# Kernel optimization log

Hardware: AMD Instinct MI355X
Metric: run time of the kernel (lower is better)

Reference implementation:

```python
import jax, jax.numpy as jnp
import numpy as np


def setup_inputs() -> dict:
    key = jax.random.key(0)
    kx, kq, kk, kv = jax.random.split(key, 4)
    B, S, D_IN, H, D_OUT = 2, 2048, 768, 12, 64
    scale = 0.02
    return {
        "x": jax.random.normal(kx, (B, S, D_IN), dtype=jnp.float32),
        "Wq": jax.random.normal(kq, (H, D_IN, D_OUT), dtype=jnp.float32) * scale,
        "Wk": jax.random.normal(kk, (H, D_IN, D_OUT), dtype=jnp.float32) * scale,
        "Wv": jax.random.normal(kv, (H, D_IN, D_OUT), dtype=jnp.float32) * scale,
    }


def reference(x, Wq, Wk, Wv):
    # x: [B, S, d_in]; Wq/Wk/Wv: [H, d_in, d_out] (stacked per-head Linear weights, no bias)
    B, S, _ = x.shape
    H, _, d_out = Wq.shape
    q = jnp.einsum("bsd,hde->bhse", x, Wq)  # [B, H, S, d_out]
    k = jnp.einsum("bsd,hde->bhse", x, Wk)
    v = jnp.einsum("bsd,hde->bhse", x, Wv)
    scores = jnp.einsum("bhse,bhte->bhst", q, k) / jnp.sqrt(jnp.float32(d_out))
    causal = jnp.tril(jnp.ones((S, S), dtype=bool))  # True = keep
    scores = jnp.where(causal, scores, jnp.float32(-jnp.inf))
    attn = jax.nn.softmax(scores, axis=-1)  # dropout = 0.0 -> identity
    ctx = jnp.einsum("bhst,bhte->bhse", attn, v)  # [B, H, S, d_out]
    # concat heads along last dim: [B, S, H*d_out]
    return ctx.transpose(0, 2, 1, 3).reshape(B, S, H * d_out)
```

## Files before the change

kernel.cpp:

```cpp
#include <hip/hip_runtime.h>
#include <hip/hip_bf16.h>


typedef short bf16x8 __attribute__((ext_vector_type(8)));
typedef short bf16x4 __attribute__((ext_vector_type(4)));
typedef float f32x4  __attribute__((ext_vector_type(4)));

#define MFMA16(a, b, c)  __builtin_amdgcn_mfma_f32_16x16x32_bf16((a), (b), (c), 0, 0, 0)
#define MFMAK16(a, b, c) __builtin_amdgcn_mfma_f32_16x16x16bf16_1k((a), (b), (c), 0, 0, 0)

static __device__ __forceinline__ unsigned short f2bf(float f) {
    unsigned int u = __builtin_bit_cast(unsigned int, f);
    u += 0x7fffu + ((u >> 16) & 1u);
    return (unsigned short)(u >> 16);
}

static __device__ __forceinline__ int sw(int row, int cb) {
    return (row << 7) + (cb ^ ((row & 7) << 4));
}

static __device__ __forceinline__ void gld16(const void* g, void* l) {
    __builtin_amdgcn_global_load_lds(
        (__attribute__((address_space(1))) void*)g,
        (__attribute__((address_space(3))) void*)l, 16, 0, 0);
}

__global__ __launch_bounds__(256) void prep(const float* __restrict__ x,
                                            const float* __restrict__ Wq,
                                            const float* __restrict__ Wk,
                                            const float* __restrict__ Wv,
                                            char* __restrict__ xb,
                                            char* __restrict__ wtb) {
    __shared__ float tile[64][65];
    const int bid = blockIdx.x;
    const int t = threadIdx.x;
    if (bid < 768) {
        const int stile = bid & 63, ks = bid >> 6;
        const int row = t >> 2, k16 = (t & 3) * 16;
        const float* src = x + (size_t)(stile * 64 + row) * 768 + ks * 64 + k16;
        char* img = xb + ((size_t)stile * 12 + ks) * 8192;
        const float4 v0 = *(const float4*)(src);
        const float4 v1 = *(const float4*)(src + 4);
        const float4 v2 = *(const float4*)(src + 8);
        const float4 v3 = *(const float4*)(src + 12);
        bf16x8 o0, o1;
        o0[0] = (short)f2bf(v0.x); o0[1] = (short)f2bf(v0.y);
        o0[2] = (short)f2bf(v0.z); o0[3] = (short)f2bf(v0.w);
        o0[4] = (short)f2bf(v1.x); o0[5] = (short)f2bf(v1.y);
        o0[6] = (short)f2bf(v1.z); o0[7] = (short)f2bf(v1.w);
        o1[0] = (short)f2bf(v2.x); o1[1] = (short)f2bf(v2.y);
        o1[2] = (short)f2bf(v2.z); o1[3] = (short)f2bf(v2.w);
        o1[4] = (short)f2bf(v3.x); o1[5] = (short)f2bf(v3.y);
        o1[6] = (short)f2bf(v3.z); o1[7] = (short)f2bf(v3.w);
        *(bf16x8*)(img + sw(row, k16 * 2)) = o0;
        *(bf16x8*)(img + sw(row, k16 * 2 + 16)) = o1;
    } else {
        const int idx = bid - 768;
        const int wh = idx % 36, dt = idx / 36;
        const int w = wh / 12, h = wh % 12;
        const float* W = (w == 0) ? Wq : (w == 1) ? Wk : Wv;
        for (int i = 0; i < 4; ++i) {
            int c = t + i * 256;
            int d = c >> 4, e4 = (c & 15) * 4;
            const float4 v = *(const float4*)(W + (size_t)(h * 768 + dt * 64 + d) * 64 + e4);
            tile[d][e4 + 0] = v.x; tile[d][e4 + 1] = v.y;
            tile[d][e4 + 2] = v.z; tile[d][e4 + 3] = v.w;
        }
        __syncthreads();
        char* img = wtb + ((size_t)(wh * 12) + dt) * 8192;
        for (int i = 0; i < 4; ++i) {
            int c = t + i * 256;
            int e = c >> 4, d4 = (c & 15) * 4;
            ushort4 o;
            o.x = f2bf(tile[d4 + 0][e]); o.y = f2bf(tile[d4 + 1][e]);
            o.z = f2bf(tile[d4 + 2][e]); o.w = f2bf(tile[d4 + 3][e]);
            *(ushort4*)(img + e * 128 + ((d4 * 2) ^ ((e & 7) << 4))) = o;
        }
    }
}

__global__ __launch_bounds__(256) void proj_qkv(const char* __restrict__ xb,
                                                const char* __restrict__ wtb,
                                                unsigned short* __restrict__ q,
                                                unsigned short* __restrict__ ksw,
                                                char* __restrict__ vsw) {
    __shared__ __align__(16) char smem[65536];
    const int stile = blockIdx.x;
    const int h = blockIdx.y;
    const int t = threadIdx.x;
    const int wave = t >> 6, lane = t & 63;
    const int lhi = lane >> 4, llo = lane & 15;
    const int wr = wave >> 1, wc = wave & 1;

    const char* asrc = xb + (size_t)stile * 12 * 8192;

    f32x4 acc[3][2][2] = {};

    #define STAGE(KS, BUF)                                                       \
        do {                                                                     \
            const char* s0 = asrc + (KS) * 8192;                                 \
            char* d0 = smem + (BUF) * 32768;                                     \
            gld16(s0 + t * 16, d0 + t * 16);                                     \
            gld16(s0 + t * 16 + 4096, d0 + t * 16 + 4096);                       \
            for (int w3 = 0; w3 < 3; ++w3) {                                     \
                const char* s1 = wtb + ((size_t)((w3 * 12 + h) * 12) + (KS)) * 8192; \
                char* d1 = smem + (BUF) * 32768 + (1 + w3) * 8192;               \
                gld16(s1 + t * 16, d1 + t * 16);                                 \
                gld16(s1 + t * 16 + 4096, d1 + t * 16 + 4096);                   \
            }                                                                    \
        } while (0)

    STAGE(0, 0);
    __syncthreads();
    int cur = 0;
    for (int ks = 0; ks < 12; ++ks) {
        if (ks < 11) STAGE(ks + 1, cur ^ 1);
        char* Alds = smem + cur * 32768;
        #pragma unroll
        for (int kk = 0; kk < 2; ++kk) {
            bf16x8 a[2];
            #pragma unroll
            for (int m = 0; m < 2; ++m)
                a[m] = *(const bf16x8*)(Alds + sw(wr * 32 + m * 16 + llo, kk * 64 + lhi * 16));
            #pragma unroll
            for (int w3 = 0; w3 < 3; ++w3) {
                char* Blds = Alds + (1 + w3) * 8192;
                #pragma unroll
                for (int n = 0; n < 2; ++n) {
                    bf16x8 b = *(const bf16x8*)(Blds + sw(wc * 32 + n * 16 + llo, kk * 64 + lhi * 16));
                    #pragma unroll
                    for (int m = 0; m < 2; ++m)
                        acc[w3][m][n] = MFMA16(a[m], b, acc[w3][m][n]);
                }
            }
        }
        __syncthreads();
        cur ^= 1;
    }
    #undef STAGE

    const float SCALE_Q = 0.18033688011112042f;
    const int bglob = stile >> 5, ktile = stile & 31;
    const int bh = bglob * 12 + h;
    #pragma unroll
    for (int m = 0; m < 2; ++m)
        for (int n = 0; n < 2; ++n)
            for (int r = 0; r < 4; ++r) {
                int s = (stile * 64 + wr * 32 + m * 16 + lhi * 4 + r) & 2047;
                int e = wc * 32 + n * 16 + llo;
                q[(size_t)(bh * 2048 + s) * 64 + e] = f2bf(acc[0][m][n][r] * SCALE_Q);
            }
    unsigned short* kdst = ksw + ((size_t)bh * 32 + ktile) * 4096;
    #pragma unroll
    for (int m = 0; m < 2; ++m)
        for (int n = 0; n < 2; ++n)
            for (int r = 0; r < 4; ++r) {
                int kk = wr * 32 + m * 16 + lhi * 4 + r;
                int e = wc * 32 + n * 16 + llo;
                kdst[kk * 64 + (e ^ ((kk & 7) << 3))] = f2bf(acc[1][m][n][r]);
            }
    char* vtimg = smem;
    __syncthreads();
    #pragma unroll
    for (int m = 0; m < 2; ++m)
        for (int n = 0; n < 2; ++n)
            for (int r = 0; r < 4; ++r) {
                int kk = wr * 32 + m * 16 + lhi * 4 + r;
                int e = wc * 32 + n * 16 + llo;
                int pos = (((kk >> 2) & 3) * 32 + (kk >> 4) * 8 + (kk & 3) * 2) ^ ((e & 7) << 4);
                *(unsigned short*)(vtimg + e * 128 + pos) = f2bf(acc[2][m][n][r]);
            }
    __syncthreads();
    {
        char* dst = vsw + ((size_t)bh * 32 + ktile) * 8192;
        #pragma unroll
        for (int i = 0; i < 2; ++i)
            *(float4*)(dst + t * 16 + i * 4096) =
                *(const float4*)(vtimg + t * 16 + i * 4096);
    }
}

__global__ __launch_bounds__(256) void attn(const unsigned short* __restrict__ Q,
                                            const char* __restrict__ Ksw,
                                            const char* __restrict__ Vsw,
                                            float* __restrict__ out) {
    __shared__ __align__(16) char smem[32768];
    const int t = threadIdx.x, wave = t >> 6, lane = t & 63;
    const int lhi = lane >> 4, llo = lane & 15;
    const int bid = blockIdx.x;
    int pt, bh;
    if (bid < 256) {
        pt = 15 - bid / 24; bh = bid % 24;
    } else {
        int i = bid - 256;
        if (i < 120) { pt = i / 24; bh = i % 24; }
        else         { pt = 5; bh = 16 + (i - 120); }
    }
    const unsigned short* Qg = Q + (size_t)bh * 2048 * 64;
    const char* Kg = Ksw + (size_t)bh * 32 * 8192;
    const char* Vg = Vsw + (size_t)bh * 32 * 8192;

    const int q0w = pt * 128 + wave * 32;
    const int ktmax_w = 2 * pt + (wave >> 1);
    const int ktlast = 2 * pt + 1;

    bf16x8 qa[2][2];
    #pragma unroll
    for (int g = 0; g < 2; ++g)
        #pragma unroll
        for (int kk = 0; kk < 2; ++kk)
            qa[g][kk] = *(const bf16x8*)(Qg + (size_t)(q0w + g * 16 + llo) * 64 + kk * 32 + lhi * 8);

    f32x4 acc[2][4] = {};
    float m_r[2] = {-1e30f, -1e30f}, l_r[2] = {0.f, 0.f};

    #define ASTAGE(KT, BUF)                                              \
        do {                                                             \
            const char* ks_ = Kg + (size_t)(KT) * 8192;                  \
            const char* vs_ = Vg + (size_t)(KT) * 8192;                  \
            char* kd = smem + (BUF) * 8192;                              \
            char* vd = smem + 16384 + (BUF) * 8192;                      \
            gld16(ks_ + t * 16, kd + t * 16);                            \
            gld16(ks_ + t * 16 + 4096, kd + t * 16 + 4096);              \
            gld16(vs_ + t * 16, vd + t * 16);                            \
            gld16(vs_ + t * 16 + 4096, vd + t * 16 + 4096);              \
        } while (0)

    ASTAGE(0, 0);
    __syncthreads();
    int cur = 0;
    for (int kt = 0; kt <= ktlast; ++kt) {
        if (kt < ktlast) ASTAGE(kt + 1, cur ^ 1);
        if (kt <= ktmax_w) {
            char* Kb = smem + cur * 8192;
            char* Vb = smem + 16384 + cur * 8192;

            f32x4 sc[2][4] = {};
            __builtin_amdgcn_s_setprio(1);
            #pragma unroll
            for (int n = 0; n < 4; ++n) {
                #pragma unroll
                for (int kk = 0; kk < 2; ++kk) {
                    bf16x8 bk = *(const bf16x8*)(Kb + sw(n * 16 + llo, kk * 64 + lhi * 16));
                    sc[0][n] = MFMA16(bk, qa[0][kk], sc[0][n]);
                    sc[1][n] = MFMA16(bk, qa[1][kk], sc[1][n]);
                }
            }
            __builtin_amdgcn_s_setprio(0);
            if (kt == ktmax_w) {
                #pragma unroll
                for (int g = 0; g < 2; ++g)
                    #pragma unroll
                    for (int n = 0; n < 4; ++n)
                        #pragma unroll
                        for (int r = 0; r < 4; ++r)
                            if (kt * 64 + n * 16 + lhi * 4 + r > q0w + g * 16 + llo)
                                sc[g][n][r] = -1e30f;
            }
            float pmax[2];
            #pragma unroll
            for (int g = 0; g < 2; ++g)
                pmax[g] = fmaxf(
                    fmaxf(fmaxf(fmaxf(sc[g][0][0], sc[g][0][1]), fmaxf(sc[g][0][2], sc[g][0][3])),
                          fmaxf(fmaxf(sc[g][1][0], sc[g][1][1]), fmaxf(sc[g][1][2], sc[g][1][3]))),
                    fmaxf(fmaxf(fmaxf(sc[g][2][0], sc[g][2][1]), fmaxf(sc[g][2][2], sc[g][2][3])),
                          fmaxf(fmaxf(sc[g][3][0], sc[g][3][1]), fmaxf(sc[g][3][2], sc[g][3][3]))));
            if (__any(pmax[0] > m_r[0] + 8.0f || pmax[1] > m_r[1] + 8.0f)) {
                #pragma unroll
                for (int g = 0; g < 2; ++g) {
                    float tm = fmaxf(pmax[g], __shfl_xor(pmax[g], 16, 64));
                    tm = fmaxf(tm, __shfl_xor(tm, 32, 64));
                    float nm = fmaxf(m_r[g], tm);
                    float corr = exp2f(m_r[g] - nm);
                    m_r[g] = nm;
                    l_r[g] *= corr;
                    #pragma unroll
                    for (int n = 0; n < 4; ++n)
                        #pragma unroll
                        for (int r = 0; r < 4; ++r) acc[g][n][r] *= corr;
                }
            }
            bf16x4 pf[2][4];
            #pragma unroll
            for (int g = 0; g < 2; ++g) {
                float ps = 0.f;
                #pragma unroll
                for (int kb = 0; kb < 4; ++kb) {
                    float p0 = exp2f(sc[g][kb][0] - m_r[g]), p1 = exp2f(sc[g][kb][1] - m_r[g]);
                    float p2 = exp2f(sc[g][kb][2] - m_r[g]), p3 = exp2f(sc[g][kb][3] - m_r[g]);
                    ps += (p0 + p1) + (p2 + p3);
                    unsigned int w0, w1;
                    asm("v_cvt_pk_bf16_f32 %0, %1, %2" : "=v"(w0) : "v"(p0), "v"(p1));
                    asm("v_cvt_pk_bf16_f32 %0, %1, %2" : "=v"(w1) : "v"(p2), "v"(p3));
                    unsigned long long u = ((unsigned long long)w1 << 32) | w0;
                    pf[g][kb] = __builtin_bit_cast(bf16x4, u);
                }
                l_r[g] += ps;
            }
            __builtin_amdgcn_s_setprio(1);
            #pragma unroll
            for (int n = 0; n < 4; ++n) {
                const int row = n * 16 + llo;
                bf16x8 v8a = *(const bf16x8*)(Vb + sw(row, lhi * 32));
                bf16x8 v8b = *(const bf16x8*)(Vb + sw(row, lhi * 32 + 16));
                bf16x4 vf0 = __builtin_shufflevector(v8a, v8a, 0, 1, 2, 3);
                bf16x4 vf1 = __builtin_shufflevector(v8a, v8a, 4, 5, 6, 7);
                bf16x4 vf2 = __builtin_shufflevector(v8b, v8b, 0, 1, 2, 3);
                bf16x4 vf3 = __builtin_shufflevector(v8b, v8b, 4, 5, 6, 7);
                #pragma unroll
                for (int g = 0; g < 2; ++g) {
                    f32x4 a = acc[g][n];
                    a = MFMAK16(vf0, pf[g][0], a);
                    a = MFMAK16(vf1, pf[g][1], a);
                    a = MFMAK16(vf2, pf[g][2], a);
                    a = MFMAK16(vf3, pf[g][3], a);
                    acc[g][n] = a;
                }
            }
            __builtin_amdgcn_s_setprio(0);
        }
        __syncthreads();
        cur ^= 1;
    }
    #undef ASTAGE
    const int b = bh / 12, h = bh - b * 12;
    #pragma unroll
    for (int g = 0; g < 2; ++g) {
        float lr = l_r[g];
        lr += __shfl_xor(lr, 16, 64);
        lr += __shfl_xor(lr, 32, 64);
        const float inv = 1.0f / lr;
        const int qrow = q0w + g * 16 + llo;
        #pragma unroll
        for (int n = 0; n < 4; ++n) {
            float4 o;
            o.x = acc[g][n][0] * inv; o.y = acc[g][n][1] * inv;
            o.z = acc[g][n][2] * inv; o.w = acc[g][n][3] * inv;
            *(float4*)(out + (size_t)(b * 2048 + qrow) * 768 + h * 64 + n * 16 + lhi * 4) = o;
        }
    }
}

extern "C" void kernel_launch(void* const* d_in, const int* in_sizes, int n_in,
                              void* d_out, int out_size, void* d_ws, size_t ws_size,
                              hipStream_t stream) {
    const float* x  = (const float*)d_in[0];
    const float* Wq = (const float*)d_in[1];
    const float* Wk = (const float*)d_in[2];
    const float* Wv = (const float*)d_in[3];
    float* out = (float*)d_out;

    char* ws = (char*)d_ws;
    char*           wtb = ws;
    unsigned short* q   = (unsigned short*)(ws + 3538944);
    unsigned short* ksw = (unsigned short*)(ws + 9830400);
    char*           vsw = (char*)(ws + 16121856);
    char*           xb  = (char*)(ws + 22413312);

    hipLaunchKernelGGL(prep, dim3(1200), dim3(256), 0, stream, x, Wq, Wk, Wv, xb, wtb);
    hipLaunchKernelGGL(proj_qkv, dim3(64, 12), dim3(256), 0, stream,
                       xb, wtb, q, ksw, vsw);
    hipLaunchKernelGGL(attn, dim3(384), dim3(256), 0, stream, q, (const char*)ksw, vsw, out);
}
```

Before: 83.45 us.

## Split long causal query tiles across KV chunks and add combine kernel

Query tiles at pt>=4 are split into KV partitions of up to 8 key tiles each. The attention grid grows from 384 to 960 blocks, so the long causal rows no longer dominate the tail and load balance across CUs improves. Each split block writes unnormalized partial outputs plus its running max and sum to workspace, and a new combine kernel merges them with log-sum-exp weights. The per-iteration __syncthreads is also replaced by explicit vmcnt waits and raw s_barrier with scheduling fences. The cost is an extra kernel launch and extra global traffic for the partial results.

```diff
diff --git a/kernel.cpp b/kernel.cpp
--- a/kernel.cpp
+++ b/kernel.cpp
@@ -8,6 +8,8 @@
 
 #define MFMA16(a, b, c)  __builtin_amdgcn_mfma_f32_16x16x32_bf16((a), (b), (c), 0, 0, 0)
 #define MFMAK16(a, b, c) __builtin_amdgcn_mfma_f32_16x16x16bf16_1k((a), (b), (c), 0, 0, 0)
+#define SCHED_FENCE() __builtin_amdgcn_sched_barrier(0)
+#define MEMBAR() asm volatile("s_barrier" ::: "memory")
 
 static __device__ __forceinline__ unsigned short f2bf(float f) {
     unsigned int u = __builtin_bit_cast(unsigned int, f);
@@ -183,33 +185,42 @@
 __global__ __launch_bounds__(256) void attn(const unsigned short* __restrict__ Q,
                                             const char* __restrict__ Ksw,
                                             const char* __restrict__ Vsw,
-                                            float* __restrict__ out) {
+                                            float* __restrict__ out,
+                                            float* __restrict__ Obuf,
+                                            float* __restrict__ mlbuf) {
     __shared__ __align__(16) char smem[32768];
     const int t = threadIdx.x, wave = t >> 6, lane = t & 63;
     const int lhi = lane >> 4, llo = lane & 15;
     const int bid = blockIdx.x;
-    int pt, bh;
-    if (bid < 256) {
-        pt = 15 - bid / 24; bh = bid % 24;
-    } else {
-        int i = bid - 256;
-        if (i < 120) { pt = i / 24; bh = i % 24; }
-        else         { pt = 5; bh = 16 + (i - 120); }
-    }
+    const int j = bid / 24, bh = bid % 24;
+    int pt, p;
+    if (j < 24) {
+        if (j < 4)       { pt = 15; p = j; }
+        else if (j < 16) { int i = j - 4;  pt = 14 - i / 3; p = i % 3; }
+        else             { int i = j - 16; pt = 10 - i / 2; p = i % 2; }
+    } else if (j < 28) { pt = 6 - (j - 24); p = 0; }
+    else {
+        int grp = (j - 28) >> 2, i = (j - 28) & 3;
+        pt = (14 - grp) - 4 * i;
+        p = 3 - i;
+    }
+    const bool split = (pt >= 4);
+    const int kts = p * 8;
+    const int kteB = min(p * 8 + 7, 2 * pt + 1);
+    const int ktmax_w = 2 * pt + (wave >> 1);
+    const int kteW = min(kteB, ktmax_w);
+
     const unsigned short* Qg = Q + (size_t)bh * 2048 * 64;
     const char* Kg = Ksw + (size_t)bh * 32 * 8192;
     const char* Vg = Vsw + (size_t)bh * 32 * 8192;
 
-    const int q0w = pt * 128 + wave * 32;
-    const int ktmax_w = 2 * pt + (wave >> 1);
-    const int ktlast = 2 * pt + 1;
-
+    const int q0 = pt * 128 + wave * 32;
     bf16x8 qa[2][2];
     #pragma unroll
     for (int g = 0; g < 2; ++g)
         #pragma unroll
         for (int kk = 0; kk < 2; ++kk)
-            qa[g][kk] = *(const bf16x8*)(Qg + (size_t)(q0w + g * 16 + llo) * 64 + kk * 32 + lhi * 8);
+            qa[g][kk] = *(const bf16x8*)(Qg + (size_t)(q0 + g * 16 + llo) * 64 + kk * 32 + lhi * 8);
 
     f32x4 acc[2][4] = {};
     float m_r[2] = {-1e30f, -1e30f}, l_r[2] = {0.f, 0.f};
@@ -226,12 +237,17 @@
             gld16(vs_ + t * 16 + 4096, vd + t * 16 + 4096);              \
         } while (0)
 
-    ASTAGE(0, 0);
-    __syncthreads();
+    ASTAGE(kts, 0);
+    SCHED_FENCE();
     int cur = 0;
-    for (int kt = 0; kt <= ktlast; ++kt) {
-        if (kt < ktlast) ASTAGE(kt + 1, cur ^ 1);
-        if (kt <= ktmax_w) {
+    for (int kt = kts; kt <= kteB; ++kt) {
+        if (kt < kteB) ASTAGE(kt + 1, cur ^ 1);
+        SCHED_FENCE();
+        if (kt < kteB) asm volatile("s_waitcnt vmcnt(4)" ::: "memory");
+        else           asm volatile("s_waitcnt vmcnt(0)" ::: "memory");
+        MEMBAR();
+        SCHED_FENCE();
+        if (kt <= kteW) {
             char* Kb = smem + cur * 8192;
             char* Vb = smem + 16384 + cur * 8192;
 
@@ -254,7 +270,7 @@
                     for (int n = 0; n < 4; ++n)
                         #pragma unroll
                         for (int r = 0; r < 4; ++r)
-                            if (kt * 64 + n * 16 + lhi * 4 + r > q0w + g * 16 + llo)
+                            if (kt * 64 + n * 16 + lhi * 4 + r > q0 + g * 16 + llo)
                                 sc[g][n][r] = -1e30f;
             }
             float pmax[2];
@@ -319,26 +335,92 @@
             }
             __builtin_amdgcn_s_setprio(0);
         }
-        __syncthreads();
+        SCHED_FENCE();
+        if (kt < kteB) MEMBAR();
         cur ^= 1;
     }
     #undef ASTAGE
+    const int off = (pt < 8) ? (pt - 4) * 2 : (pt < 12) ? 8 + (pt - 8) * 3 : 20 + (pt - 12) * 4;
     const int b = bh / 12, h = bh - b * 12;
     #pragma unroll
     for (int g = 0; g < 2; ++g) {
         float lr = l_r[g];
         lr += __shfl_xor(lr, 16, 64);
         lr += __shfl_xor(lr, 32, 64);
-        const float inv = 1.0f / lr;
-        const int qrow = q0w + g * 16 + llo;
+        if (split) {
+            const int slot = bh * 36 + off + p;
+            float* Ob = Obuf + (size_t)slot * 8192;
+            const int qrow = wave * 32 + g * 16 + llo;
+            #pragma unroll
+            for (int n = 0; n < 4; ++n) {
+                float4 o;
+                o.x = acc[g][n][0]; o.y = acc[g][n][1];
+                o.z = acc[g][n][2]; o.w = acc[g][n][3];
+                *(float4*)(Ob + qrow * 64 + n * 16 + lhi * 4) = o;
+            }
+            if (lhi == 0) {
+                float2 ml; ml.x = m_r[g]; ml.y = lr;
+                *(float2*)(mlbuf + (size_t)slot * 256 + qrow * 2) = ml;
+            }
+        } else {
+            const float inv = 1.0f / lr;
+            const int qrow = q0 + g * 16 + llo;
+            #pragma unroll
+            for (int n = 0; n < 4; ++n) {
+                float4 o;
+                o.x = acc[g][n][0] * inv; o.y = acc[g][n][1] * inv;
+                o.z = acc[g][n][2] * inv; o.w = acc[g][n][3] * inv;
+                *(float4*)(out + (size_t)(b * 2048 + qrow) * 768 + h * 64 + n * 16 + lhi * 4) = o;
+            }
+        }
+    }
+}
+
+__global__ __launch_bounds__(256) void combine(const float* __restrict__ Obuf,
+                                               const float* __restrict__ mlbuf,
+                                               float* __restrict__ out) {
+    const int bid = blockIdx.x;
+    const int bh = bid % 24, pt = 4 + bid / 24;
+    const int np = (pt < 8) ? 2 : (pt < 12) ? 3 : 4;
+    const int off = (pt < 8) ? (pt - 4) * 2 : (pt < 12) ? 8 + (pt - 8) * 3 : 20 + (pt - 12) * 4;
+    const int base = bh * 36 + off;
+    const int b = bh / 12, h = bh - b * 12;
+    const int t = threadIdx.x;
+    const int r = t >> 1, c0 = (t & 1) * 32;
+
+    float m[4], l[4];
+    float mm = -1e30f;
+    for (int i = 0; i < np; ++i) {
+        float2 ml = *(const float2*)(mlbuf + (size_t)(base + i) * 256 + r * 2);
+        m[i] = ml.x; l[i] = ml.y;
+        mm = fmaxf(mm, ml.x);
+    }
+    float L = 0.f, w[4];
+    for (int i = 0; i < np; ++i) { w[i] = exp2f(m[i] - mm); L += l[i] * w[i]; }
+    const float inv = 1.0f / L;
+
+    float4 o[8];
+    {
+        const float* s = Obuf + (size_t)base * 8192 + r * 64 + c0;
+        const float wi = w[0] * inv;
         #pragma unroll
-        for (int n = 0; n < 4; ++n) {
-            float4 o;
-            o.x = acc[g][n][0] * inv; o.y = acc[g][n][1] * inv;
-            o.z = acc[g][n][2] * inv; o.w = acc[g][n][3] * inv;
-            *(float4*)(out + (size_t)(b * 2048 + qrow) * 768 + h * 64 + n * 16 + lhi * 4) = o;
-        }
-    }
+        for (int k = 0; k < 8; ++k) {
+            float4 a = *(const float4*)(s + k * 4);
+            o[k].x = a.x * wi; o[k].y = a.y * wi; o[k].z = a.z * wi; o[k].w = a.w * wi;
+        }
+    }
+    for (int i = 1; i < np; ++i) {
+        const float* s = Obuf + (size_t)(base + i) * 8192 + r * 64 + c0;
+        const float wi = w[i] * inv;
+        #pragma unroll
+        for (int k = 0; k < 8; ++k) {
+            float4 a = *(const float4*)(s + k * 4);
+            o[k].x += a.x * wi; o[k].y += a.y * wi; o[k].z += a.z * wi; o[k].w += a.w * wi;
+        }
+    }
+    float* dst = out + (size_t)(b * 2048 + pt * 128 + r) * 768 + h * 64 + c0;
+    #pragma unroll
+    for (int k = 0; k < 8; ++k) *(float4*)(dst + k * 4) = o[k];
 }
 
 extern "C" void kernel_launch(void* const* d_in, const int* in_sizes, int n_in,
@@ -351,14 +433,18 @@
     float* out = (float*)d_out;
 
     char* ws = (char*)d_ws;
-    char*           wtb = ws;
-    unsigned short* q   = (unsigned short*)(ws + 3538944);
-    unsigned short* ksw = (unsigned short*)(ws + 9830400);
-    char*           vsw = (char*)(ws + 16121856);
-    char*           xb  = (char*)(ws + 22413312);
+    char*           wtb   = ws;
+    unsigned short* q     = (unsigned short*)(ws + 3538944);
+    unsigned short* ksw   = (unsigned short*)(ws + 9830400);
+    char*           vsw   = (char*)(ws + 16121856);
+    char*           xb    = (char*)(ws + 22413312);
+    float*          Obuf  = (float*)(ws + 28704768);
+    float*          mlbuf = (float*)(ws + 57016320);
 
     hipLaunchKernelGGL(prep, dim3(1200), dim3(256), 0, stream, x, Wq, Wk, Wv, xb, wtb);
     hipLaunchKernelGGL(proj_qkv, dim3(64, 12), dim3(256), 0, stream,
                        xb, wtb, q, ksw, vsw);
-    hipLaunchKernelGGL(attn, dim3(384), dim3(256), 0, stream, q, (const char*)ksw, vsw, out);
-}
+    hipLaunchKernelGGL(attn, dim3(960), dim3(256), 0, stream,
+                       q, (const char*)ksw, vsw, out, Obuf, mlbuf);
+    hipLaunchKernelGGL(combine, dim3(288), dim3(256), 0, stream, Obuf, mlbuf, out);
+}
```

Result: faster. 80.78 us (-3.2%).
